# Performance work log

Hardware: AMD Instinct MI355X
Metric: run time of the kernel (lower is better)

## Reference

```python
import jax, jax.numpy as jnp
import numpy as np
from jax import lax

B, T, C = 2, 1024, 2048
H, N = 32, 64
LAYER_ID, N_LAYER = 1, 24
EPS = 1e-5 * 64.0  # 1e-5 * head_size_divisor**2, divisor=8
RESCALE_T = 256.0 * 0.7  # bf16_limit * 0.7


def setup_inputs():
    key = jax.random.key(0)
    ks = jax.random.split(key, 16)
    r01 = LAYER_ID / (N_LAYER - 1)
    r10 = 1.0 - LAYER_ID / N_LAYER
    ddd = np.arange(C, dtype=np.float64) / C
    pw = lambda p: jnp.asarray(1.0 - ddd ** p, jnp.float32)
    n = np.arange(C, dtype=np.float64)
    decay = -7.0 + 5.0 * (n / (C - 1)) ** (0.85 + r01 ** 0.5)
    sc = lambda k, shp, s: jax.random.normal(k, shp, jnp.float32) * s
    return {
        'x': sc(ks[0], (B, T, C), 1.0),
        'v_first': sc(ks[1], (B, T, C), 1.0),
        'x_r': pw(0.2 * r10), 'x_w': pw(0.9 * r10),
        'x_k': jnp.asarray(1.0 - (ddd ** (0.9 * r10) + 0.4 * r01), jnp.float32),
        'x_v': jnp.asarray(1.0 - (ddd ** (0.4 * r10) + 0.6 * r01), jnp.float32),
        'x_a': pw(0.9 * r10), 'x_g': pw(0.2 * r10),
        'w0': jnp.asarray(decay + 0.5, jnp.float32),
        'w1': sc(ks[2], (C, 64), 0.02), 'w2': sc(ks[3], (64, C), 0.02),
        'a0': jnp.zeros((C,), jnp.float32),
        'a1': sc(ks[4], (C, 64), 0.02), 'a2': sc(ks[5], (64, C), 0.02),
        'v0': jnp.ones((C,), jnp.float32),
        'v1': sc(ks[6], (C, 32), 0.02), 'v2': sc(ks[7], (32, C), 0.02),
        'g1': sc(ks[8], (C, 128), 0.02), 'g2': sc(ks[9], (128, C), 0.02),
        'k_k': jnp.full((C,), 0.85, jnp.float32),
        'k_a': jnp.ones((C,), jnp.float32),
        'r_k': sc(ks[10], (H, N), 0.05),
        'W_r': sc(ks[11], (C, C), C ** -0.5),
        'W_k': sc(ks[12], (C, C), C ** -0.5),
        'W_v': sc(ks[13], (C, C), C ** -0.5),
        'W_o': sc(ks[14], (C, C), C ** -0.5),
        'ln_w': jnp.ones((C,), jnp.float32),
        'ln_b': jnp.zeros((C,), jnp.float32),
    }


def wkv7(r, w, k, v, a, b):
    # RWKV-7 per-head linear state recurrence: S <- S*diag(w) + S a b^T + v k^T; out = S r
    Bsz, Tlen, Cd = r.shape
    to = lambda t: t.reshape(Bsz, Tlen, H, N).transpose(1, 0, 2, 3)  # (T,B,H,N)
    rr, kk, vv, aa, bb = map(to, (r, k, v, a, b))
    ww = jnp.exp(-jnp.exp(to(w)))  # decay in (0,1); w <= -0.5 guaranteed upstream

    def step(S, xs):
        rt, wt, kt, vt, at, bt = xs
        sa = jnp.einsum('bhij,bhj->bhi', S, at)
        S = S * wt[:, :, None, :] + sa[..., None] * bt[:, :, None, :] + vt[..., None] * kt[:, :, None, :]
        return S, jnp.einsum('bhij,bhj->bhi', S, rt)

    S0 = jnp.zeros((Bsz, H, N, N), r.dtype)
    _, out = lax.scan(step, S0, (rr, ww, kk, vv, aa, bb))
    return out.transpose(1, 0, 2, 3).reshape(Bsz, Tlen, Cd)


def reference(x, v_first, x_r, x_w, x_k, x_v, x_a, x_g, w0, w1, w2, a0, a1, a2,
              v0, v1, v2, g1, g2, k_k, k_a, r_k, W_r, W_k, W_v, W_o, ln_w, ln_b):
    # token shift (ZeroPad2d((0,0,1,-1)))
    xx = jnp.concatenate([jnp.zeros_like(x[:, :1]), x[:, :-1]], axis=1) - x
    xr = x + xx * x_r; xw = x + xx * x_w; xk = x + xx * x_k
    xv = x + xx * x_v; xa = x + xx * x_a; xg = x + xx * x_g
    r = xr @ W_r.T
    w = -jax.nn.softplus(-(w0 + jnp.tanh(xw @ w1) @ w2)) - 0.5  # soft clamp to (-inf,-0.5]
    k = xk @ W_k.T
    v = xv @ W_v.T
    # layer_id > 0: value residual gated toward v_first (with max-abs rescales)
    v1p = xv @ v1
    v1p = v1p / jnp.maximum(jnp.max(jnp.abs(v1p)), 1.0)
    v2p = v1p @ v2
    v2p = v2p / jnp.maximum(jnp.max(jnp.abs(v2p)), 1.0)
    gate = jax.nn.sigmoid(jnp.clip(v0 + v2p, -16.0, 16.0))
    vd = v_first - v
    vd = vd / jnp.maximum(jnp.max(jnp.abs(vd)), 1.0)
    v = v + vd * gate
    a = jax.nn.sigmoid(a0 + (xa @ a1) @ a2)
    g = jax.nn.sigmoid(xg @ g1) @ g2
    kk = (k * k_k).reshape(B, T, H, N)
    kk = (kk / jnp.maximum(jnp.linalg.norm(kk, axis=-1, keepdims=True), 1e-12)).reshape(B, T, C)
    k = k * (1.0 + (a - 1.0) * k_a)
    y = wkv7(r, w, k, v, -kk, kk * a)
    needs_rescale = jnp.max(jnp.abs(y)) > RESCALE_T
    # GroupNorm: H groups of size N
    yg = y.reshape(B, T, H, N)
    mu = yg.mean(-1, keepdims=True)
    var = yg.var(-1, keepdims=True)
    y = ((yg - mu) / jnp.sqrt(var + EPS)).reshape(B, T, C) * ln_w + ln_b
    y = y + ((r.reshape(B, T, H, N) * k.reshape(B, T, H, N) * r_k).sum(-1, keepdims=True)
             * v.reshape(B, T, H, N)).reshape(B, T, C)
    y = (y * g) @ W_o.T
    y = jnp.where(needs_rescale, y * 0.5, y)
    v_first_out = jnp.where(needs_rescale, v_first * 0.5, v_first)
    return y, v_first_out
```

## Files before the change

kernel.cpp:

```cpp
#include <hip/hip_runtime.h>
#include <hip/hip_bf16.h>

#define ELq 4194304
#define Cq 2048
#define Tq 1024
#define Hq 32
#define Mq 2048

typedef __attribute__((ext_vector_type(8))) short bf16x8;
typedef __attribute__((ext_vector_type(4))) float f32x4;

__device__ __forceinline__ unsigned short f2bu(float f) {
  union { float f; unsigned u; } v; v.f = f;
  unsigned r = v.u + 0x7fffu + ((v.u >> 16) & 1u);
  return (unsigned short)(r >> 16);
}
__device__ __forceinline__ float b2f(unsigned short u) {
  union { unsigned u; float f; } v; v.u = ((unsigned)u) << 16;
  return v.f;
}
__device__ __forceinline__ void gl_lds16(const void* g, void* l) {
  __builtin_amdgcn_global_load_lds((const __attribute__((address_space(1))) unsigned int*)g,
                                   (__attribute__((address_space(3))) unsigned int*)l, 16, 0, 0);
}

template<int CTRL>
__device__ __forceinline__ float dpp_add(float x) {
  int t = __builtin_amdgcn_update_dpp(0, __builtin_bit_cast(int, x), CTRL, 0xF, 0xF, true);
  return x + __builtin_bit_cast(float, t);
}

__device__ __forceinline__ float4 b4f(uint2 u) {
  float4 f;
  f.x = __uint_as_float(u.x << 16);
  f.y = __uint_as_float(u.x & 0xffff0000u);
  f.z = __uint_as_float(u.y << 16);
  f.w = __uint_as_float(u.y & 0xffff0000u);
  return f;
}

struct ConvJob { const float* src; unsigned short* dst; int rows, cols, trans; };
struct ConvJobs { ConvJob j[12]; unsigned int* scal; };

__global__ void k_conv(ConvJobs jobs) {
  if (blockIdx.z == 0 && blockIdx.x == 0 && threadIdx.x < 8) jobs.scal[threadIdx.x] = 0u;
  ConvJob jb = jobs.j[blockIdx.z];
  int n = jb.rows * jb.cols;
  if (!jb.trans) {
    int n4 = n >> 2;
    for (int i = blockIdx.x * blockDim.x + threadIdx.x; i < n4; i += gridDim.x * blockDim.x) {
      float4 v = ((const float4*)jb.src)[i];
      ushort4 o;
      o.x = f2bu(v.x); o.y = f2bu(v.y); o.z = f2bu(v.z); o.w = f2bu(v.w);
      ((ushort4*)jb.dst)[i] = o;
    }
  } else {
    for (int i = blockIdx.x * blockDim.x + threadIdx.x; i < n; i += gridDim.x * blockDim.x) {
      int col = i / jb.rows;
      int row = i - col * jb.rows;
      jb.dst[i] = f2bu(jb.src[(size_t)row * jb.cols + col]);
    }
  }
}

__global__ void k_prologue(const float* __restrict__ x,
    const float* __restrict__ mr, const float* __restrict__ mw, const float* __restrict__ mk,
    const float* __restrict__ mv, const float* __restrict__ ma, const float* __restrict__ mg,
    unsigned short* __restrict__ xr, unsigned short* __restrict__ xw, unsigned short* __restrict__ xk,
    unsigned short* __restrict__ xv, unsigned short* __restrict__ xa, unsigned short* __restrict__ xg)
{
  int i4 = blockIdx.x * 256 + threadIdx.x;
  if (i4 >= ELq / 4) return;
  int i = i4 << 2;
  float4 xc = *(const float4*)(x + i);
  int t = (i >> 11) & (Tq - 1);
  float4 xp = make_float4(0.f, 0.f, 0.f, 0.f);
  if (t) xp = *(const float4*)(x + i - Cq);
  float4 dx = make_float4(xp.x - xc.x, xp.y - xc.y, xp.z - xc.z, xp.w - xc.w);
  int c = i & (Cq - 1);
  auto mix = [&](const float* __restrict__ m, unsigned short* __restrict__ o) {
    float4 mm = *(const float4*)(m + c);
    ushort4 u;
    u.x = f2bu(xc.x + dx.x * mm.x); u.y = f2bu(xc.y + dx.y * mm.y);
    u.z = f2bu(xc.z + dx.z * mm.z); u.w = f2bu(xc.w + dx.w * mm.w);
    *(ushort4*)(o + i) = u;
  };
  mix(mr, xr); mix(mw, xw); mix(mk, xk); mix(mv, xv); mix(ma, xa); mix(mg, xg);
}

struct GJob {
  const unsigned short* A; const unsigned short* B;
  const float* bias; float* Cf; unsigned short* Cb;
  unsigned int* amax; const float* aux;
  int K; int ld; int epi;
  const float* kkw; const float* kaw;
  unsigned short* kk16; unsigned short* bb16; const float* asig;
};
struct GJobs { GJob j[4]; };

__device__ __forceinline__ void epi_store(int epi, float v, size_t o,
    float* Cf, unsigned short* Cb, const float* bias, const float* aux, int col, float& lmax)
{
  switch (epi) {
    case 0: Cf[o] = v; break;
    case 1: Cf[o] = v + bias[col]; break;
    case 2: Cf[o] = 1.f / (1.f + expf(-(v + bias[col]))); break;
    case 4: Cb[o] = f2bu(v); break;
    case 7: lmax = fmaxf(lmax, fabsf(v)); Cf[o] = v; break;
    case 9: lmax = fmaxf(lmax, fabsf(aux[o] - v)); Cf[o] = v; break;
    case 10: {
      float wv = v + bias[col];
      float wlog = -log1pf(expf(-wv)) - 0.5f;
      Cf[o] = expf(-expf(wlog));
      break;
    }
  }
}

__global__ __launch_bounds__(256, 2) void k_gemm128(GJobs jobs) {
  GJob jb = jobs.j[blockIdx.z];
  __shared__ __align__(16) unsigned short As[128 * 32];
  __shared__ __align__(16) unsigned short Bs[128 * 32];
  __shared__ float sred[4];
  const int tid = threadIdx.x, lane = tid & 63, wid = tid >> 6;
  const int wr = wid >> 1, wc = wid & 1;
  const int lin = blockIdx.y * 16 + blockIdx.x;
  const int swz = (lin & 7) * 32 + (lin >> 3);
  const int m0 = (swz >> 4) * 128, n0 = (swz & 15) * 128;
  const int K = jb.K, ld = jb.ld;
  const unsigned short* A = jb.A; const unsigned short* B = jb.B;
  f32x4 acc[4][4] = {};
  for (int k0 = 0; k0 < K; k0 += 32) {
    #pragma unroll
    for (int i = 0; i < 2; ++i) {
      int cw = wid * 64 + i * 256;
      int c = cw + lane;
      int row = c >> 2, q = c & 3;
      gl_lds16(A + (size_t)(m0 + row) * ld + k0 + q * 8, &As[cw * 8]);
      gl_lds16(B + (size_t)(n0 + row) * ld + k0 + q * 8, &Bs[cw * 8]);
    }
    __syncthreads();
    const int kg = (lane >> 4) * 8;
    bf16x8 af[4], bq[4];
    #pragma unroll
    for (int mi = 0; mi < 4; ++mi)
      af[mi] = *(const bf16x8*)&As[(wr * 64 + mi * 16 + (lane & 15)) * 32 + kg];
    #pragma unroll
    for (int ni = 0; ni < 4; ++ni)
      bq[ni] = *(const bf16x8*)&Bs[(wc * 64 + ni * 16 + (lane & 15)) * 32 + kg];
    #pragma unroll
    for (int mi = 0; mi < 4; ++mi)
      #pragma unroll
      for (int ni = 0; ni < 4; ++ni)
        acc[mi][ni] = __builtin_amdgcn_mfma_f32_16x16x32_bf16(af[mi], bq[ni], acc[mi][ni], 0, 0, 0);
    __syncthreads();
  }
  if (jb.epi == 11) {
    float kkwv[4], kawv[4]; int colv[4];
    #pragma unroll
    for (int ni = 0; ni < 4; ++ni) {
      colv[ni] = n0 + wc * 64 + ni * 16 + (lane & 15);
      kkwv[ni] = jb.kkw[colv[ni]];
      kawv[ni] = jb.kaw[colv[ni]];
    }
    #pragma unroll
    for (int mi = 0; mi < 4; ++mi) {
      #pragma unroll
      for (int q = 0; q < 4; ++q) {
        float kkv[4]; float ss = 0.f;
        #pragma unroll
        for (int ni = 0; ni < 4; ++ni) {
          kkv[ni] = acc[mi][ni][q] * kkwv[ni];
          ss += kkv[ni] * kkv[ni];
        }
        ss = dpp_add<0xB1>(ss); ss = dpp_add<0x4E>(ss);
        ss = dpp_add<0x141>(ss); ss = dpp_add<0x140>(ss);
        float inv = 1.f / fmaxf(sqrtf(ss), 1e-12f);
        int row = m0 + wr * 64 + mi * 16 + ((lane >> 4) << 2) + q;
        #pragma unroll
        for (int ni = 0; ni < 4; ++ni) {
          size_t o = (size_t)row * 2048 + colv[ni];
          float kraw = acc[mi][ni][q];
          float kkn = kkv[ni] * inv;
          float as = jb.asig[o];
          jb.kk16[o] = f2bu(-kkn);
          jb.bb16[o] = f2bu(kkn * as);
          jb.Cb[o] = f2bu(kraw * (1.f + (as - 1.f) * kawv[ni]));
        }
      }
    }
    return;
  }
  float lmax = 0.f;
  #pragma unroll
  for (int mi = 0; mi < 4; ++mi)
    #pragma unroll
    for (int ni = 0; ni < 4; ++ni) {
      int col = n0 + wc * 64 + ni * 16 + (lane & 15);
      int row = m0 + wr * 64 + mi * 16 + ((lane >> 4) << 2);
      #pragma unroll
      for (int q = 0; q < 4; ++q)
        epi_store(jb.epi, acc[mi][ni][q], (size_t)(row + q) * 2048 + col,
                  jb.Cf, jb.Cb, jb.bias, jb.aux, col, lmax);
    }
  if (jb.epi == 7 || jb.epi == 9) {
    #pragma unroll
    for (int o = 32; o; o >>= 1) lmax = fmaxf(lmax, __shfl_xor(lmax, o));
    if (lane == 0) sred[wid] = lmax;
    __syncthreads();
    if (tid == 0)
      atomicMax(jb.amax, __float_as_uint(fmaxf(fmaxf(sred[0], sred[1]), fmaxf(sred[2], sred[3]))));
  }
}

template<int TBN>
__device__ __forceinline__ void sk_body(const GJob& jb,
    unsigned short* __restrict__ As, unsigned short* __restrict__ Bs) {
  const int tid = threadIdx.x, lane = tid & 63, wid = tid >> 6;
  const int m0 = blockIdx.x * 128;
  const int koff = blockIdx.y * 256;
  const int ld = jb.ld;
  constexpr int NF = TBN / 16;
  const unsigned short* A = jb.A + koff;
  const unsigned short* B = jb.B + koff;
  float* out = jb.Cf + (size_t)blockIdx.y * (2048 * TBN);
  f32x4 acc[2][NF] = {};
  for (int k0 = 0; k0 < 256; k0 += 32) {
    for (int cw = wid * 64; cw < 512; cw += 256) {
      int c = cw + lane; int row = c >> 2, q = c & 3;
      gl_lds16(A + (size_t)(m0 + row) * ld + k0 + q * 8, &As[cw * 8]);
    }
    for (int cw = wid * 64; cw < TBN * 4; cw += 256) {
      int c = cw + lane; int row = c >> 2, q = c & 3;
      gl_lds16(B + (size_t)row * ld + k0 + q * 8, &Bs[cw * 8]);
    }
    __syncthreads();
    const int kg = (lane >> 4) * 8;
    bf16x8 af[2], bq[NF];
    #pragma unroll
    for (int mi = 0; mi < 2; ++mi)
      af[mi] = *(const bf16x8*)&As[(wid * 32 + mi * 16 + (lane & 15)) * 32 + kg];
    #pragma unroll
    for (int ni = 0; ni < NF; ++ni)
      bq[ni] = *(const bf16x8*)&Bs[(ni * 16 + (lane & 15)) * 32 + kg];
    #pragma unroll
    for (int mi = 0; mi < 2; ++mi)
      #pragma unroll
      for (int ni = 0; ni < NF; ++ni)
        acc[mi][ni] = __builtin_amdgcn_mfma_f32_16x16x32_bf16(af[mi], bq[ni], acc[mi][ni], 0, 0, 0);
    __syncthreads();
  }
  #pragma unroll
  for (int mi = 0; mi < 2; ++mi)
    #pragma unroll
    for (int ni = 0; ni < NF; ++ni) {
      int col = ni * 16 + (lane & 15);
      int row = m0 + wid * 32 + mi * 16 + ((lane >> 4) << 2);
      #pragma unroll
      for (int q = 0; q < 4; ++q)
        out[(size_t)(row + q) * TBN + col] = acc[mi][ni][q];
    }
}

__global__ __launch_bounds__(256, 2) void k_skinny(GJobs jobs) {
  __shared__ __align__(16) unsigned short As[128 * 32];
  __shared__ __align__(16) unsigned short Bs[128 * 32];
  switch (blockIdx.z) {
    case 0:  sk_body<64>(jobs.j[0], As, Bs); break;
    case 1:  sk_body<64>(jobs.j[1], As, Bs); break;
    case 2:  sk_body<32>(jobs.j[2], As, Bs); break;
    default: sk_body<128>(jobs.j[3], As, Bs); break;
  }
}

__global__ void k_skepi(const float* __restrict__ pw, const float* __restrict__ pa,
                        const float* __restrict__ pv, const float* __restrict__ pg,
                        unsigned short* __restrict__ hw, unsigned short* __restrict__ ha,
                        unsigned short* __restrict__ hv, unsigned short* __restrict__ hg,
                        unsigned int* __restrict__ amax) {
  int i = blockIdx.x * 256 + threadIdx.x;
  const float* src; unsigned short* dst; int stride, mode, loc;
  if (i < 131072)      { src = pw; dst = hw; stride = 131072; mode = 0; loc = i; }
  else if (i < 262144) { src = pa; dst = ha; stride = 131072; mode = 1; loc = i - 131072; }
  else if (i < 327680) { src = pv; dst = hv; stride = 65536;  mode = 2; loc = i - 262144; }
  else                 { src = pg; dst = hg; stride = 262144; mode = 3; loc = i - 327680; }
  float s = 0.f;
  #pragma unroll
  for (int sp = 0; sp < 8; ++sp) s += src[loc + (size_t)sp * stride];
  float lmax = 0.f, o;
  switch (mode) {
    case 0: o = tanhf(s); break;
    case 1: o = s; break;
    case 2: o = s; lmax = fabsf(s); break;
    default: o = 1.f / (1.f + expf(-s)); break;
  }
  dst[loc] = f2bu(o);
  #pragma unroll
  for (int of = 32; of; of >>= 1) lmax = fmaxf(lmax, __shfl_xor(lmax, of));
  if ((threadIdx.x & 63) == 0 && lmax > 0.f) atomicMax(amax, __float_as_uint(lmax));
}

__global__ void k_vfin(float* __restrict__ v, const float* __restrict__ vf,
                       const float* __restrict__ z, const float* __restrict__ v0c,
                       const unsigned int* __restrict__ sc) {
  int i4 = blockIdx.x * 256 + threadIdx.x;
  if (i4 >= ELq / 4) return;
  int i = i4 << 2;
  float m1 = fmaxf(__uint_as_float(sc[0]), 1.f);
  float m2 = fmaxf(__uint_as_float(sc[1]) / m1, 1.f);
  float inv12 = 1.f / (m1 * m2);
  float invvd = 1.f / fmaxf(__uint_as_float(sc[2]), 1.f);
  int c = i & (Cq - 1);
  float4 zv = *(const float4*)(z + i);
  float4 vv = *(const float4*)(v + i);
  float4 fv = *(const float4*)(vf + i);
  float4 v0v = *(const float4*)(v0c + c);
  float4 o;
  #pragma unroll
  for (int j = 0; j < 4; ++j) {
    float gx = (&v0v.x)[j] + (&zv.x)[j] * inv12;
    gx = fminf(fmaxf(gx, -16.f), 16.f);
    float gate = 1.f / (1.f + expf(-gx));
    float vr = (&vv.x)[j];
    (&o.x)[j] = vr + ((&fv.x)[j] - vr) * (gate * invvd);
  }
  *(float4*)(v + i) = o;
}

struct SRg { uint2 r, k, a, b; float4 w; float v; };

__device__ __forceinline__ void ld_g(SRg& R,
    const unsigned short* __restrict__ rS, const float* __restrict__ wS,
    const unsigned short* __restrict__ kS, const float* __restrict__ vS,
    const unsigned short* __restrict__ aS, const unsigned short* __restrict__ bS,
    size_t sb, int cl, int row) {
  R.r = *(const uint2*)(rS + sb + cl);
  R.k = *(const uint2*)(kS + sb + cl);
  R.a = *(const uint2*)(aS + sb + cl);
  R.b = *(const uint2*)(bS + sb + cl);
  R.w = *(const float4*)(wS + sb + cl);
  R.v = vS[sb + row];
}

__device__ __forceinline__ void wkv_step(const SRg& R, float S[4], float& ymx,
    float* __restrict__ y, size_t yoff, int lane) {
  float4 av = b4f(R.a);
  float sa = (S[0]*av.x + S[1]*av.y) + (S[2]*av.z + S[3]*av.w);
  sa = dpp_add<0xB1>(sa);
  sa = dpp_add<0x4E>(sa);
  sa = dpp_add<0x141>(sa);
  sa = dpp_add<0x140>(sa);
  float4 kv = b4f(R.k), bv = b4f(R.b), rv = b4f(R.r);
  float vi = R.v;
  float s0 = S[0]*R.w.x + (sa*bv.x + vi*kv.x);
  float s1 = S[1]*R.w.y + (sa*bv.y + vi*kv.y);
  float s2 = S[2]*R.w.z + (sa*bv.z + vi*kv.z);
  float s3 = S[3]*R.w.w + (sa*bv.w + vi*kv.w);
  S[0]=s0; S[1]=s1; S[2]=s2; S[3]=s3;
  float yp = (s0*rv.x + s1*rv.y) + (s2*rv.z + s3*rv.w);
  yp = dpp_add<0xB1>(yp);
  yp = dpp_add<0x4E>(yp);
  yp = dpp_add<0x141>(yp);
  yp = dpp_add<0x140>(yp);
  if ((lane & 15) == 0) {
    y[yoff] = yp;
    ymx = fmaxf(ymx, fabsf(yp));
  }
}

__global__ __launch_bounds__(64, 1) void k_wkv(
    const unsigned short* __restrict__ rS, const float* __restrict__ wS,
    const unsigned short* __restrict__ kS, const float* __restrict__ vS,
    const unsigned short* __restrict__ aS, const unsigned short* __restrict__ bS,
    float* __restrict__ y, unsigned int* __restrict__ ymax) {
  const int lane = threadIdx.x;
  const int bh = blockIdx.x & 63;
  const int rq = blockIdx.x >> 6;
  const int row = rq * 4 + (lane >> 4);
  const int cl = (lane & 15) * 4;
  float S[4];
  #pragma unroll
  for (int q = 0; q < 4; ++q) S[q] = 0.f;
  const size_t base0 = (size_t)(bh >> 5) * Tq * Cq + (size_t)(bh & 31) * 64;

  SRg R0, R1, R2, R3, R4, R5, R6, R7;
  ld_g(R0, rS, wS, kS, vS, aS, bS, base0,          cl, row);
  ld_g(R1, rS, wS, kS, vS, aS, bS, base0 + Cq,     cl, row);
  ld_g(R2, rS, wS, kS, vS, aS, bS, base0 + 2 * Cq, cl, row);
  ld_g(R3, rS, wS, kS, vS, aS, bS, base0 + 3 * Cq, cl, row);
  ld_g(R4, rS, wS, kS, vS, aS, bS, base0 + 4 * Cq, cl, row);
  ld_g(R5, rS, wS, kS, vS, aS, bS, base0 + 5 * Cq, cl, row);
  ld_g(R6, rS, wS, kS, vS, aS, bS, base0 + 6 * Cq, cl, row);
  ld_g(R7, rS, wS, kS, vS, aS, bS, base0 + 7 * Cq, cl, row);

  float ymx = 0.f;
  for (int t = 0; t < Tq; t += 8) {
    int n0 = (t + 8  < Tq) ? t + 8  : Tq - 1;
    int n1 = (t + 9  < Tq) ? t + 9  : Tq - 1;
    int n2 = (t + 10 < Tq) ? t + 10 : Tq - 1;
    int n3 = (t + 11 < Tq) ? t + 11 : Tq - 1;
    int n4 = (t + 12 < Tq) ? t + 12 : Tq - 1;
    int n5 = (t + 13 < Tq) ? t + 13 : Tq - 1;
    int n6 = (t + 14 < Tq) ? t + 14 : Tq - 1;
    int n7 = (t + 15 < Tq) ? t + 15 : Tq - 1;
    wkv_step(R0, S, ymx, y, base0 + (size_t)t * Cq + row, lane);
    ld_g(R0, rS, wS, kS, vS, aS, bS, base0 + (size_t)n0 * Cq, cl, row);
    wkv_step(R1, S, ymx, y, base0 + (size_t)(t + 1) * Cq + row, lane);
    ld_g(R1, rS, wS, kS, vS, aS, bS, base0 + (size_t)n1 * Cq, cl, row);
    wkv_step(R2, S, ymx, y, base0 + (size_t)(t + 2) * Cq + row, lane);
    ld_g(R2, rS, wS, kS, vS, aS, bS, base0 + (size_t)n2 * Cq, cl, row);
    wkv_step(R3, S, ymx, y, base0 + (size_t)(t + 3) * Cq + row, lane);
    ld_g(R3, rS, wS, kS, vS, aS, bS, base0 + (size_t)n3 * Cq, cl, row);
    wkv_step(R4, S, ymx, y, base0 + (size_t)(t + 4) * Cq + row, lane);
    ld_g(R4, rS, wS, kS, vS, aS, bS, base0 + (size_t)n4 * Cq, cl, row);
    wkv_step(R5, S, ymx, y, base0 + (size_t)(t + 5) * Cq + row, lane);
    ld_g(R5, rS, wS, kS, vS, aS, bS, base0 + (size_t)n5 * Cq, cl, row);
    wkv_step(R6, S, ymx, y, base0 + (size_t)(t + 6) * Cq + row, lane);
    ld_g(R6, rS, wS, kS, vS, aS, bS, base0 + (size_t)n6 * Cq, cl, row);
    wkv_step(R7, S, ymx, y, base0 + (size_t)(t + 7) * Cq + row, lane);
    ld_g(R7, rS, wS, kS, vS, aS, bS, base0 + (size_t)n7 * Cq, cl, row);
  }
  #pragma unroll
  for (int o = 32; o; o >>= 1) ymx = fmaxf(ymx, __shfl_xor(ymx, o));
  if (lane == 0) atomicMax(ymax, __float_as_uint(ymx));
}

__global__ __launch_bounds__(256) void k_epi1(const float* __restrict__ y,
    const unsigned short* __restrict__ r, const unsigned short* __restrict__ k,
    const float* __restrict__ v, const unsigned short* __restrict__ g,
    const float* __restrict__ lnw, const float* __restrict__ lnb, const float* __restrict__ rk,
    unsigned short* __restrict__ yg) {
  int wid = threadIdx.x >> 6, lane = threadIdx.x & 63;
  int idx = blockIdx.x * 4 + wid;
  size_t off = (size_t)idx * 64 + lane;
  int c = ((idx & (Hq - 1)) << 6) | lane;
  float yv = y[off];
  float s = yv;
  #pragma unroll
  for (int o = 32; o; o >>= 1) s += __shfl_xor(s, o);
  float mu = s * (1.f / 64.f);
  float d = yv - mu;
  float vs = d * d;
  #pragma unroll
  for (int o = 32; o; o >>= 1) vs += __shfl_xor(vs, o);
  float yn = d / sqrtf(vs * (1.f / 64.f) + 6.4e-4f);
  float yo = yn * lnw[c] + lnb[c];
  float bon = b2f(r[off]) * b2f(k[off]) * rk[c];
  #pragma unroll
  for (int o = 32; o; o >>= 1) bon += __shfl_xor(bon, o);
  yo += bon * v[off];
  yg[off] = f2bu(yo * b2f(g[off]));
}

__global__ void k_fin(const float* __restrict__ p0, const float* __restrict__ p1,
                      const unsigned int* __restrict__ sc, float* __restrict__ yout,
                      const float* __restrict__ vf, float* __restrict__ vfout) {
  int i = blockIdx.x * 256 + threadIdx.x;
  float s = (__uint_as_float(sc[3]) > 179.2f) ? 0.5f : 1.f;
  if (i < ELq / 4) {
    float4 a = ((const float4*)p0)[i];
    float4 b = ((const float4*)p1)[i];
    ((float4*)yout)[i] = make_float4((a.x + b.x) * s, (a.y + b.y) * s,
                                     (a.z + b.z) * s, (a.w + b.w) * s);
  } else {
    int j = i - ELq / 4;
    float4 vv = ((const float4*)vf)[j];
    ((float4*)vfout)[j] = make_float4(vv.x * s, vv.y * s, vv.z * s, vv.w * s);
  }
}

extern "C" void kernel_launch(void* const* d_in, const int* in_sizes, int n_in,
                              void* d_out, int out_size, void* d_ws, size_t ws_size,
                              hipStream_t stream) {
  const float* x      = (const float*)d_in[0];
  const float* vfirst = (const float*)d_in[1];
  const float* x_r = (const float*)d_in[2];
  const float* x_w = (const float*)d_in[3];
  const float* x_k = (const float*)d_in[4];
  const float* x_v = (const float*)d_in[5];
  const float* x_a = (const float*)d_in[6];
  const float* x_g = (const float*)d_in[7];
  const float* w0 = (const float*)d_in[8];
  const float* w1 = (const float*)d_in[9];
  const float* w2 = (const float*)d_in[10];
  const float* a0 = (const float*)d_in[11];
  const float* a1 = (const float*)d_in[12];
  const float* a2 = (const float*)d_in[13];
  const float* v0 = (const float*)d_in[14];
  const float* v1 = (const float*)d_in[15];
  const float* v2 = (const float*)d_in[16];
  const float* g1 = (const float*)d_in[17];
  const float* g2 = (const float*)d_in[18];
  const float* k_k = (const float*)d_in[19];
  const float* k_a = (const float*)d_in[20];
  const float* r_k = (const float*)d_in[21];
  const float* W_r = (const float*)d_in[22];
  const float* W_k = (const float*)d_in[23];
  const float* W_v = (const float*)d_in[24];
  const float* W_o = (const float*)d_in[25];
  const float* lnw = (const float*)d_in[26];
  const float* lnb = (const float*)d_in[27];

  char* ws = (char*)d_ws;
  size_t off = 0;
  auto alloc = [&](size_t bytes) -> void* {
    void* p = ws + off; off += (bytes + 255) & ~(size_t)255; return p;
  };
  unsigned int* scal = (unsigned int*)alloc(256);
  float* vbuf  = (float*)alloc((size_t)ELq * 4);
  float* wbuf  = (float*)alloc((size_t)ELq * 4);
  float* abuf  = (float*)alloc((size_t)ELq * 4);
  float* ybuf  = (float*)alloc((size_t)ELq * 4);
  unsigned short* rb16 = (unsigned short*)alloc((size_t)ELq * 2);
  unsigned short* kb16 = (unsigned short*)alloc((size_t)ELq * 2);
  unsigned short* kk16 = (unsigned short*)alloc((size_t)ELq * 2);
  unsigned short* bb16 = (unsigned short*)alloc((size_t)ELq * 2);
  unsigned short* xrb = (unsigned short*)alloc((size_t)ELq * 2);
  unsigned short* xwb = (unsigned short*)alloc((size_t)ELq * 2);
  unsigned short* xkb = (unsigned short*)alloc((size_t)ELq * 2);
  unsigned short* xvb = (unsigned short*)alloc((size_t)ELq * 2);
  unsigned short* xab = (unsigned short*)alloc((size_t)ELq * 2);
  unsigned short* xgb = (unsigned short*)alloc((size_t)ELq * 2);
  unsigned short* gbuf = (unsigned short*)alloc((size_t)ELq * 2);
  unsigned short* ygb  = (unsigned short*)alloc((size_t)ELq * 2);
  unsigned short* WrB = (unsigned short*)alloc((size_t)ELq * 2);
  unsigned short* WkB = (unsigned short*)alloc((size_t)ELq * 2);
  unsigned short* WvB = (unsigned short*)alloc((size_t)ELq * 2);
  unsigned short* WoB = (unsigned short*)alloc((size_t)ELq * 2);
  unsigned short* w1T = (unsigned short*)alloc(64 * 2048 * 2);
  unsigned short* a1T = (unsigned short*)alloc(64 * 2048 * 2);
  unsigned short* v1T = (unsigned short*)alloc(32 * 2048 * 2);
  unsigned short* g1T = (unsigned short*)alloc(128 * 2048 * 2);
  unsigned short* w2T = (unsigned short*)alloc(2048 * 64 * 2);
  unsigned short* a2T = (unsigned short*)alloc(2048 * 64 * 2);
  unsigned short* v2T = (unsigned short*)alloc(2048 * 32 * 2);
  unsigned short* g2T = (unsigned short*)alloc(2048 * 128 * 2);
  unsigned short* hwb = (unsigned short*)alloc((size_t)Mq * 64 * 2);
  unsigned short* hab = (unsigned short*)alloc((size_t)Mq * 64 * 2);
  unsigned short* hvb = (unsigned short*)alloc((size_t)Mq * 32 * 2);
  unsigned short* hgb = (unsigned short*)alloc((size_t)Mq * 128 * 2);
  float* pskw = (float*)alloc((size_t)8 * Mq * 64 * 4);
  float* pska = (float*)alloc((size_t)8 * Mq * 64 * 4);
  float* pskv = (float*)alloc((size_t)8 * Mq * 32 * 4);
  float* pskg = (float*)alloc((size_t)8 * Mq * 128 * 4);
  float* zbuf = (float*)d_out + ELq;
  float* yout = (float*)d_out;
  float* vfout = (float*)d_out + ELq;
  float* pWo0 = (float*)xrb;
  float* pWo1 = pWo0 + ELq;

  ConvJobs cj;
  cj.j[0]  = {W_r, WrB, Cq, Cq, 0};
  cj.j[1]  = {W_k, WkB, Cq, Cq, 0};
  cj.j[2]  = {W_v, WvB, Cq, Cq, 0};
  cj.j[3]  = {W_o, WoB, Cq, Cq, 0};
  cj.j[4]  = {w1, w1T, 2048, 64, 1};
  cj.j[5]  = {a1, a1T, 2048, 64, 1};
  cj.j[6]  = {v1, v1T, 2048, 32, 1};
  cj.j[7]  = {g1, g1T, 2048, 128, 1};
  cj.j[8]  = {w2, w2T, 64, 2048, 1};
  cj.j[9]  = {a2, a2T, 64, 2048, 1};
  cj.j[10] = {v2, v2T, 32, 2048, 1};
  cj.j[11] = {g2, g2T, 128, 2048, 1};
  cj.scal = scal;
  k_conv<<<dim3(1024, 1, 12), 256, 0, stream>>>(cj);

  k_prologue<<<ELq / 1024, 256, 0, stream>>>(x, x_r, x_w, x_k, x_v, x_a, x_g,
                                             xrb, xwb, xkb, xvb, xab, xgb);

  GJobs gsk;
  gsk.j[0] = {xwb, w1T, nullptr, pskw, nullptr, nullptr, nullptr, 256, 2048, 0};
  gsk.j[1] = {xab, a1T, nullptr, pska, nullptr, nullptr, nullptr, 256, 2048, 0};
  gsk.j[2] = {xvb, v1T, nullptr, pskv, nullptr, nullptr, nullptr, 256, 2048, 0};
  gsk.j[3] = {xgb, g1T, nullptr, pskg, nullptr, nullptr, nullptr, 256, 2048, 0};
  k_skinny<<<dim3(16, 8, 4), 256, 0, stream>>>(gsk);
  k_skepi<<<2304, 256, 0, stream>>>(pskw, pska, pskv, pskg, hwb, hab, hvb, hgb, scal + 0);

  GJobs g3j;
  g3j.j[0] = {hwb, w2T, w0, wbuf, nullptr, nullptr, nullptr, 64, 64, 10};
  g3j.j[1] = {hab, a2T, a0, abuf, nullptr, nullptr, nullptr, 64, 64, 2};
  g3j.j[2] = {hvb, v2T, nullptr, zbuf, nullptr, scal + 1, nullptr, 32, 32, 7};
  g3j.j[3] = {hgb, g2T, nullptr, nullptr, gbuf, nullptr, nullptr, 128, 128, 4};
  k_gemm128<<<dim3(16, 16, 4), 256, 0, stream>>>(g3j);

  GJobs g1j;
  g1j.j[0] = {xrb, WrB, nullptr, nullptr, rb16, nullptr, nullptr, 2048, 2048, 4};
  g1j.j[1] = {xkb, WkB, nullptr, nullptr, kb16, nullptr, nullptr, 2048, 2048, 11,
              k_k, k_a, kk16, bb16, abuf};
  g1j.j[2] = {xvb, WvB, nullptr, vbuf, nullptr, scal + 2, vfirst, 2048, 2048, 9};
  g1j.j[3] = g1j.j[0];
  k_gemm128<<<dim3(16, 16, 3), 256, 0, stream>>>(g1j);

  k_vfin<<<ELq / 1024, 256, 0, stream>>>(vbuf, vfirst, zbuf, v0, scal);
  k_wkv<<<16 * 2 * Hq, 64, 0, stream>>>(rb16, wbuf, kb16, vbuf, kk16, bb16, ybuf, scal + 3);
  k_epi1<<<(2 * Tq * Hq) / 4, 256, 0, stream>>>(ybuf, rb16, kb16, vbuf, gbuf, lnw, lnb, r_k, ygb);

  GJobs gfj;
  gfj.j[0] = {ygb, WoB, nullptr, pWo0, nullptr, nullptr, nullptr, 1024, 2048, 0};
  gfj.j[1] = {ygb + 1024, WoB + 1024, nullptr, pWo1, nullptr, nullptr, nullptr, 1024, 2048, 0};
  gfj.j[2] = gfj.j[0]; gfj.j[3] = gfj.j[0];
  k_gemm128<<<dim3(16, 16, 2), 256, 0, stream>>>(gfj);
  k_fin<<<ELq / 512, 256, 0, stream>>>(pWo0, pWo1, scal, yout, vfirst, vfout);
}
```

Before: 524.6 us.

## Pack WKV inputs into per-head per-timestep 1KB slots and stage via LDS ring

The GEMM epilogues and the v-finalize kernel now write r, k, kk, b, w and v into one interleaved buffer. Each (batch, head, timestep) gets a contiguous 1KB slot, replacing six separate strided row-major arrays. The WKV scan loads each slot with a single global-to-LDS 16-byte-per-lane copy into an 8-deep shared-memory ring, replacing eight register sets of scattered loads. This aims to cut scan load latency and improve coalescing. The cost is scattered 2- and 4-byte stores in the GEMM epilogues, which may reduce their write efficiency.

```diff
diff --git a/kernel.cpp b/kernel.cpp
--- a/kernel.cpp
+++ b/kernel.cpp
@@ -37,6 +37,10 @@
   f.z = __uint_as_float(u.y << 16);
   f.w = __uint_as_float(u.y & 0xffff0000u);
   return f;
+}
+
+__device__ __forceinline__ size_t sb_off(int m, int c) {
+  return ((size_t)(((m >> 10) * 32 + (c >> 6)) * 1024 + (m & 1023))) << 10;
 }
 
 struct ConvJob { const float* src; unsigned short* dst; int rows, cols, trans; };
@@ -93,8 +97,8 @@
   const float* bias; float* Cf; unsigned short* Cb;
   unsigned int* amax; const float* aux;
   int K; int ld; int epi;
-  const float* kkw; const float* kaw;
-  unsigned short* kk16; unsigned short* bb16; const float* asig;
+  const float* kkw; const float* kaw; const float* asig;
+  unsigned char* scan;
 };
 struct GJobs { GJob j[4]; };
 
@@ -108,12 +112,6 @@
     case 4: Cb[o] = f2bu(v); break;
     case 7: lmax = fmaxf(lmax, fabsf(v)); Cf[o] = v; break;
     case 9: lmax = fmaxf(lmax, fabsf(aux[o] - v)); Cf[o] = v; break;
-    case 10: {
-      float wv = v + bias[col];
-      float wlog = -log1pf(expf(-wv)) - 0.5f;
-      Cf[o] = expf(-expf(wlog));
-      break;
-    }
   }
 }
 
@@ -154,6 +152,38 @@
       for (int ni = 0; ni < 4; ++ni)
         acc[mi][ni] = __builtin_amdgcn_mfma_f32_16x16x32_bf16(af[mi], bq[ni], acc[mi][ni], 0, 0, 0);
     __syncthreads();
+  }
+  if (jb.epi == 12) {
+    #pragma unroll
+    for (int mi = 0; mi < 4; ++mi)
+      #pragma unroll
+      for (int ni = 0; ni < 4; ++ni) {
+        int col = n0 + wc * 64 + ni * 16 + (lane & 15);
+        int row0 = m0 + wr * 64 + mi * 16 + ((lane >> 4) << 2);
+        #pragma unroll
+        for (int q = 0; q < 4; ++q)
+          *(unsigned short*)(jb.scan + sb_off(row0 + q, col) + ((col & 63) << 1)) =
+              f2bu(acc[mi][ni][q]);
+      }
+    return;
+  }
+  if (jb.epi == 10) {
+    #pragma unroll
+    for (int mi = 0; mi < 4; ++mi)
+      #pragma unroll
+      for (int ni = 0; ni < 4; ++ni) {
+        int col = n0 + wc * 64 + ni * 16 + (lane & 15);
+        int row0 = m0 + wr * 64 + mi * 16 + ((lane >> 4) << 2);
+        float bc = jb.bias[col];
+        #pragma unroll
+        for (int q = 0; q < 4; ++q) {
+          float wv = acc[mi][ni][q] + bc;
+          float wlog = -log1pf(expf(-wv)) - 0.5f;
+          *(float*)(jb.scan + sb_off(row0 + q, col) + 512 + ((col & 63) << 2)) =
+              expf(-expf(wlog));
+        }
+      }
+    return;
   }
   if (jb.epi == 11) {
     float kkwv[4], kawv[4]; int colv[4];
@@ -179,13 +209,15 @@
         int row = m0 + wr * 64 + mi * 16 + ((lane >> 4) << 2) + q;
         #pragma unroll
         for (int ni = 0; ni < 4; ++ni) {
-          size_t o = (size_t)row * 2048 + colv[ni];
+          int col = colv[ni];
+          unsigned char* base = jb.scan + sb_off(row, col);
+          int n2 = (col & 63) << 1;
           float kraw = acc[mi][ni][q];
           float kkn = kkv[ni] * inv;
-          float as = jb.asig[o];
-          jb.kk16[o] = f2bu(-kkn);
-          jb.bb16[o] = f2bu(kkn * as);
-          jb.Cb[o] = f2bu(kraw * (1.f + (as - 1.f) * kawv[ni]));
+          float as = jb.asig[(size_t)row * 2048 + col];
+          *(unsigned short*)(base + 128 + n2) = f2bu(kraw * (1.f + (as - 1.f) * kawv[ni]));
+          *(unsigned short*)(base + 256 + n2) = f2bu(-kkn);
+          *(unsigned short*)(base + 384 + n2) = f2bu(kkn * as);
         }
       }
     }
@@ -300,9 +332,9 @@
   if ((threadIdx.x & 63) == 0 && lmax > 0.f) atomicMax(amax, __float_as_uint(lmax));
 }
 
-__global__ void k_vfin(float* __restrict__ v, const float* __restrict__ vf,
+__global__ void k_vfin(const float* __restrict__ v, const float* __restrict__ vf,
                        const float* __restrict__ z, const float* __restrict__ v0c,
-                       const unsigned int* __restrict__ sc) {
+                       const unsigned int* __restrict__ sc, unsigned char* __restrict__ scan) {
   int i4 = blockIdx.x * 256 + threadIdx.x;
   if (i4 >= ELq / 4) return;
   int i = i4 << 2;
@@ -310,6 +342,7 @@
   float m2 = fmaxf(__uint_as_float(sc[1]) / m1, 1.f);
   float inv12 = 1.f / (m1 * m2);
   float invvd = 1.f / fmaxf(__uint_as_float(sc[2]), 1.f);
+  int m = i >> 11;
   int c = i & (Cq - 1);
   float4 zv = *(const float4*)(z + i);
   float4 vv = *(const float4*)(v + i);
@@ -324,22 +357,18 @@
     float vr = (&vv.x)[j];
     (&o.x)[j] = vr + ((&fv.x)[j] - vr) * (gate * invvd);
   }
-  *(float4*)(v + i) = o;
+  *(float4*)(scan + sb_off(m, c) + 768 + ((c & 63) << 2)) = o;
 }
 
 struct SRg { uint2 r, k, a, b; float4 w; float v; };
 
-__device__ __forceinline__ void ld_g(SRg& R,
-    const unsigned short* __restrict__ rS, const float* __restrict__ wS,
-    const unsigned short* __restrict__ kS, const float* __restrict__ vS,
-    const unsigned short* __restrict__ aS, const unsigned short* __restrict__ bS,
-    size_t sb, int cl, int row) {
-  R.r = *(const uint2*)(rS + sb + cl);
-  R.k = *(const uint2*)(kS + sb + cl);
-  R.a = *(const uint2*)(aS + sb + cl);
-  R.b = *(const uint2*)(bS + sb + cl);
-  R.w = *(const float4*)(wS + sb + cl);
-  R.v = vS[sb + row];
+__device__ __forceinline__ void ld_sr(SRg& R, const unsigned char* slot, int lq, int rw) {
+  R.r = *(const uint2*)(slot + lq * 8);
+  R.k = *(const uint2*)(slot + 128 + lq * 8);
+  R.a = *(const uint2*)(slot + 256 + lq * 8);
+  R.b = *(const uint2*)(slot + 384 + lq * 8);
+  R.w = *(const float4*)(slot + 512 + lq * 16);
+  R.v = *(const float*)(slot + 768 + rw * 4);
 }
 
 __device__ __forceinline__ void wkv_step(const SRg& R, float S[4], float& ymx,
@@ -368,72 +397,61 @@
   }
 }
 
-__global__ __launch_bounds__(64, 1) void k_wkv(
-    const unsigned short* __restrict__ rS, const float* __restrict__ wS,
-    const unsigned short* __restrict__ kS, const float* __restrict__ vS,
-    const unsigned short* __restrict__ aS, const unsigned short* __restrict__ bS,
+#define VMW(n) asm volatile("s_waitcnt vmcnt(" #n ")" ::: "memory")
+
+__global__ __launch_bounds__(64, 1) void k_wkv(const unsigned char* __restrict__ scan,
     float* __restrict__ y, unsigned int* __restrict__ ymax) {
   const int lane = threadIdx.x;
   const int bh = blockIdx.x & 63;
   const int rq = blockIdx.x >> 6;
   const int row = rq * 4 + (lane >> 4);
-  const int cl = (lane & 15) * 4;
+  const int lq = lane & 15;
+  __shared__ __align__(16) unsigned char ring[8][1024];
   float S[4];
   #pragma unroll
   for (int q = 0; q < 4; ++q) S[q] = 0.f;
-  const size_t base0 = (size_t)(bh >> 5) * Tq * Cq + (size_t)(bh & 31) * 64;
-
-  SRg R0, R1, R2, R3, R4, R5, R6, R7;
-  ld_g(R0, rS, wS, kS, vS, aS, bS, base0,          cl, row);
-  ld_g(R1, rS, wS, kS, vS, aS, bS, base0 + Cq,     cl, row);
-  ld_g(R2, rS, wS, kS, vS, aS, bS, base0 + 2 * Cq, cl, row);
-  ld_g(R3, rS, wS, kS, vS, aS, bS, base0 + 3 * Cq, cl, row);
-  ld_g(R4, rS, wS, kS, vS, aS, bS, base0 + 4 * Cq, cl, row);
-  ld_g(R5, rS, wS, kS, vS, aS, bS, base0 + 5 * Cq, cl, row);
-  ld_g(R6, rS, wS, kS, vS, aS, bS, base0 + 6 * Cq, cl, row);
-  ld_g(R7, rS, wS, kS, vS, aS, bS, base0 + 7 * Cq, cl, row);
-
+  const unsigned char* gs = scan + ((size_t)bh << 20);
+  const size_t ybase = (size_t)(bh >> 5) * Tq * Cq + (size_t)(bh & 31) * 64 + row;
+
+  auto stage = [&](int tt, int slot) {
+    gl_lds16(gs + ((size_t)tt << 10) + lane * 16, &ring[slot][0]);
+  };
+  stage(0, 0); stage(1, 1); stage(2, 2); stage(3, 3);
+  stage(4, 4); stage(5, 5); stage(6, 6); stage(7, 7);
+  VMW(7);
+  SRg SA, SB;
+  ld_sr(SA, ring[0], lq, row);
+  asm volatile("s_waitcnt lgkmcnt(0)" ::: "memory");
   float ymx = 0.f;
-  for (int t = 0; t < Tq; t += 8) {
-    int n0 = (t + 8  < Tq) ? t + 8  : Tq - 1;
-    int n1 = (t + 9  < Tq) ? t + 9  : Tq - 1;
-    int n2 = (t + 10 < Tq) ? t + 10 : Tq - 1;
-    int n3 = (t + 11 < Tq) ? t + 11 : Tq - 1;
-    int n4 = (t + 12 < Tq) ? t + 12 : Tq - 1;
-    int n5 = (t + 13 < Tq) ? t + 13 : Tq - 1;
-    int n6 = (t + 14 < Tq) ? t + 14 : Tq - 1;
-    int n7 = (t + 15 < Tq) ? t + 15 : Tq - 1;
-    wkv_step(R0, S, ymx, y, base0 + (size_t)t * Cq + row, lane);
-    ld_g(R0, rS, wS, kS, vS, aS, bS, base0 + (size_t)n0 * Cq, cl, row);
-    wkv_step(R1, S, ymx, y, base0 + (size_t)(t + 1) * Cq + row, lane);
-    ld_g(R1, rS, wS, kS, vS, aS, bS, base0 + (size_t)n1 * Cq, cl, row);
-    wkv_step(R2, S, ymx, y, base0 + (size_t)(t + 2) * Cq + row, lane);
-    ld_g(R2, rS, wS, kS, vS, aS, bS, base0 + (size_t)n2 * Cq, cl, row);
-    wkv_step(R3, S, ymx, y, base0 + (size_t)(t + 3) * Cq + row, lane);
-    ld_g(R3, rS, wS, kS, vS, aS, bS, base0 + (size_t)n3 * Cq, cl, row);
-    wkv_step(R4, S, ymx, y, base0 + (size_t)(t + 4) * Cq + row, lane);
-    ld_g(R4, rS, wS, kS, vS, aS, bS, base0 + (size_t)n4 * Cq, cl, row);
-    wkv_step(R5, S, ymx, y, base0 + (size_t)(t + 5) * Cq + row, lane);
-    ld_g(R5, rS, wS, kS, vS, aS, bS, base0 + (size_t)n5 * Cq, cl, row);
-    wkv_step(R6, S, ymx, y, base0 + (size_t)(t + 6) * Cq + row, lane);
-    ld_g(R6, rS, wS, kS, vS, aS, bS, base0 + (size_t)n6 * Cq, cl, row);
-    wkv_step(R7, S, ymx, y, base0 + (size_t)(t + 7) * Cq + row, lane);
-    ld_g(R7, rS, wS, kS, vS, aS, bS, base0 + (size_t)n7 * Cq, cl, row);
-  }
+
+#define WITER(WN, T, SC, SN) { \
+    VMW(WN); \
+    stage((T) + 8 < Tq ? (T) + 8 : Tq - 1, ((T) + 8) & 7); \
+    ld_sr(SN, ring[((T) + 1) & 7], lq, row); \
+    wkv_step(SC, S, ymx, y, ybase + (size_t)(T) * Cq, lane); }
+
+  WITER(6, 0, SA, SB)  WITER(7, 1, SB, SA)  WITER(8, 2, SA, SB)  WITER(9, 3, SB, SA)
+  WITER(10, 4, SA, SB) WITER(11, 5, SB, SA) WITER(12, 6, SA, SB) WITER(13, 7, SB, SA)
+  for (int t = 8; t < Tq; t += 2) {
+    WITER(13, t, SA, SB)
+    WITER(13, t + 1, SB, SA)
+  }
+#undef WITER
   #pragma unroll
   for (int o = 32; o; o >>= 1) ymx = fmaxf(ymx, __shfl_xor(ymx, o));
   if (lane == 0) atomicMax(ymax, __float_as_uint(ymx));
 }
 
 __global__ __launch_bounds__(256) void k_epi1(const float* __restrict__ y,
-    const unsigned short* __restrict__ r, const unsigned short* __restrict__ k,
-    const float* __restrict__ v, const unsigned short* __restrict__ g,
+    const unsigned char* __restrict__ scan, const unsigned short* __restrict__ g,
     const float* __restrict__ lnw, const float* __restrict__ lnb, const float* __restrict__ rk,
     unsigned short* __restrict__ yg) {
   int wid = threadIdx.x >> 6, lane = threadIdx.x & 63;
   int idx = blockIdx.x * 4 + wid;
   size_t off = (size_t)idx * 64 + lane;
   int c = ((idx & (Hq - 1)) << 6) | lane;
+  int b = idx >> 15, t = (idx >> 5) & 1023, h = idx & 31;
+  const unsigned char* so = scan + ((((size_t)(b * 32 + h)) << 10 | t) << 10);
   float yv = y[off];
   float s = yv;
   #pragma unroll
@@ -445,10 +463,13 @@
   for (int o = 32; o; o >>= 1) vs += __shfl_xor(vs, o);
   float yn = d / sqrtf(vs * (1.f / 64.f) + 6.4e-4f);
   float yo = yn * lnw[c] + lnb[c];
-  float bon = b2f(r[off]) * b2f(k[off]) * rk[c];
+  float rv = b2f(*(const unsigned short*)(so + lane * 2));
+  float kv = b2f(*(const unsigned short*)(so + 128 + lane * 2));
+  float vv = *(const float*)(so + 768 + lane * 4);
+  float bon = rv * kv * rk[c];
   #pragma unroll
   for (int o = 32; o; o >>= 1) bon += __shfl_xor(bon, o);
-  yo += bon * v[off];
+  yo += bon * vv;
   yg[off] = f2bu(yo * b2f(g[off]));
 }
 
@@ -507,14 +528,10 @@
     void* p = ws + off; off += (bytes + 255) & ~(size_t)255; return p;
   };
   unsigned int* scal = (unsigned int*)alloc(256);
+  unsigned char* scanbuf = (unsigned char*)alloc((size_t)64 * Tq * 1024);
   float* vbuf  = (float*)alloc((size_t)ELq * 4);
-  float* wbuf  = (float*)alloc((size_t)ELq * 4);
   float* abuf  = (float*)alloc((size_t)ELq * 4);
   float* ybuf  = (float*)alloc((size_t)ELq * 4);
-  unsigned short* rb16 = (unsigned short*)alloc((size_t)ELq * 2);
-  unsigned short* kb16 = (unsigned short*)alloc((size_t)ELq * 2);
-  unsigned short* kk16 = (unsigned short*)alloc((size_t)ELq * 2);
-  unsigned short* bb16 = (unsigned short*)alloc((size_t)ELq * 2);
   unsigned short* xrb = (unsigned short*)alloc((size_t)ELq * 2);
   unsigned short* xwb = (unsigned short*)alloc((size_t)ELq * 2);
   unsigned short* xkb = (unsigned short*)alloc((size_t)ELq * 2);
@@ -577,23 +594,25 @@
   k_skepi<<<2304, 256, 0, stream>>>(pskw, pska, pskv, pskg, hwb, hab, hvb, hgb, scal + 0);
 
   GJobs g3j;
-  g3j.j[0] = {hwb, w2T, w0, wbuf, nullptr, nullptr, nullptr, 64, 64, 10};
+  g3j.j[0] = {hwb, w2T, w0, nullptr, nullptr, nullptr, nullptr, 64, 64, 10,
+              nullptr, nullptr, nullptr, scanbuf};
   g3j.j[1] = {hab, a2T, a0, abuf, nullptr, nullptr, nullptr, 64, 64, 2};
   g3j.j[2] = {hvb, v2T, nullptr, zbuf, nullptr, scal + 1, nullptr, 32, 32, 7};
   g3j.j[3] = {hgb, g2T, nullptr, nullptr, gbuf, nullptr, nullptr, 128, 128, 4};
   k_gemm128<<<dim3(16, 16, 4), 256, 0, stream>>>(g3j);
 
   GJobs g1j;
-  g1j.j[0] = {xrb, WrB, nullptr, nullptr, rb16, nullptr, nullptr, 2048, 2048, 4};
-  g1j.j[1] = {xkb, WkB, nullptr, nullptr, kb16, nullptr, nullptr, 2048, 2048, 11,
-              k_k, k_a, kk16, bb16, abuf};
+  g1j.j[0] = {xrb, WrB, nullptr, nullptr, nullptr, nullptr, nullptr, 2048, 2048, 12,
+              nullptr, nullptr, nullptr, scanbuf};
+  g1j.j[1] = {xkb, WkB, nullptr, nullptr, nullptr, nullptr, nullptr, 2048, 2048, 11,
+              k_k, k_a, abuf, scanbuf};
   g1j.j[2] = {xvb, WvB, nullptr, vbuf, nullptr, scal + 2, vfirst, 2048, 2048, 9};
   g1j.j[3] = g1j.j[0];
   k_gemm128<<<dim3(16, 16, 3), 256, 0, stream>>>(g1j);
 
-  k_vfin<<<ELq / 1024, 256, 0, stream>>>(vbuf, vfirst, zbuf, v0, scal);
-  k_wkv<<<16 * 2 * Hq, 64, 0, stream>>>(rb16, wbuf, kb16, vbuf, kk16, bb16, ybuf, scal + 3);
-  k_epi1<<<(2 * Tq * Hq) / 4, 256, 0, stream>>>(ybuf, rb16, kb16, vbuf, gbuf, lnw, lnb, r_k, ygb);
+  k_vfin<<<ELq / 1024, 256, 0, stream>>>(vbuf, vfirst, zbuf, v0, scal, scanbuf);
+  k_wkv<<<16 * 2 * Hq, 64, 0, stream>>>(scanbuf, ybuf, scal + 3);
+  k_epi1<<<(2 * Tq * Hq) / 4, 256, 0, stream>>>(ybuf, scanbuf, gbuf, lnw, lnb, r_k, ygb);
 
   GJobs gfj;
   gfj.j[0] = {ygb, WoB, nullptr, pWo0, nullptr, nullptr, nullptr, 1024, 2048, 0};
```

After: 722.3 us. 1.38x slower.
